# Kernel optimization log

Hardware: AMD Instinct MI355X
Metric: run time of the kernel (lower is better)

Reference implementation:

```python
import jax, jax.numpy as jnp
import numpy as np

EMB_DIM = 300
VOCAB_X = 50000
VOCAB_Y = 50000
LEN_X = 64
LEN_Y = 64
BATCH = 1024
PAD_ID = 0


def setup_inputs() -> dict:
    key = jax.random.key(0)
    k1, k2, k3, k4, k5, k6, k7 = jax.random.split(key, 7)
    initrange = 0.5 / EMB_DIM
    emb_x = jax.random.uniform(k1, (VOCAB_X, EMB_DIM), jnp.float32, -initrange, initrange)
    emb_y = jax.random.uniform(k2, (VOCAB_Y, EMB_DIM), jnp.float32, -initrange, initrange)
    # padding row zeroed as in init_emb
    emb_x = emb_x.at[PAD_ID].set(0.0)
    emb_y = emb_y.at[PAD_ID].set(0.0)
    return {
        "samp_hid": jax.random.normal(k3, (BATCH, EMB_DIM), jnp.float32),
        "batch_x": jax.random.randint(k4, (BATCH, LEN_X), 0, VOCAB_X, jnp.int64 if jax.config.jax_enable_x64 else jnp.int32),
        "batch_y": jax.random.randint(k5, (BATCH, LEN_Y), 0, VOCAB_Y, jnp.int64 if jax.config.jax_enable_x64 else jnp.int32),
        "emb_x": emb_x,
        "emb_y": emb_y,
        "bias_x": jax.random.uniform(k6, (VOCAB_X,), jnp.float32),
        "bias_y": jax.random.uniform(k7, (VOCAB_Y,), jnp.float32),
    }


def _cal_nll(z, tokens, emb, bias):
    # logits shared across all positions: [B, V]
    logits = z @ emb.T + bias
    logp = jax.nn.log_softmax(logits, axis=-1)            # compute log-softmax ONCE per row
    tok_logp = jnp.take_along_axis(logp, tokens, axis=1)  # [B, L] gather per-position targets
    mask = (tokens != PAD_ID).astype(logits.dtype)        # CrossEntropyLoss(ignore_index=0)
    return jnp.sum(-tok_logp * mask, axis=1)              # sum over positions -> [B]


def reference(samp_hid, batch_x, batch_y, emb_x, emb_y, bias_x, bias_y):
    nll_x = _cal_nll(samp_hid, batch_x, emb_x, bias_x)
    nll_y = _cal_nll(samp_hid, batch_y, emb_y, bias_y)
    return jnp.mean(nll_x + nll_y)
```

## Files before the change

kernel.cpp:

```cpp
#include <hip/hip_runtime.h>

#define V_VOCAB 50000
#define K_DIM   300
#define NROWS   1024
#define LEN     64
#define NBC     392
#define CGS     1568
#define KS      19

typedef __attribute__((ext_vector_type(8)))  short bf16x8;
typedef __attribute__((ext_vector_type(16))) float f32x16;

static __device__ __forceinline__ unsigned short f2bf(float f) {
    unsigned int u = __builtin_bit_cast(unsigned int, f);
    u = u + 0x7fffu + ((u >> 16) & 1u);
    return (unsigned short)(u >> 16);
}

static __device__ __forceinline__ f32x16 zero16() {
    f32x16 z;
#pragma unroll
    for (int i = 0; i < 16; ++i) z[i] = 0.0f;
    return z;
}

static __device__ __forceinline__ void gload_lds16(const void* g, void* l) {
    __builtin_amdgcn_global_load_lds((const __attribute__((address_space(1))) void*)g,
                                     (__attribute__((address_space(3))) void*)l, 16, 0, 0);
}

__global__ void zbf_kernel(const float* __restrict__ z, unsigned short* __restrict__ zbf) {
    int t = blockIdx.x * 256 + threadIdx.x;
    int l    = t & 63;
    int rest = t >> 6;
    int ks   = rest % KS;
    int rblk = rest / KS;
    int row  = rblk * 32 + (l & 31);
    int k0   = ks * 16 + (l >> 5) * 8;
    unsigned short o[8];
#pragma unroll
    for (int j = 0; j < 8; ++j) {
        int k = k0 + j;
        float v = (k < K_DIM) ? z[row * K_DIM + k] : ((k == K_DIM) ? 1.0f : 0.0f);
        o[j] = f2bf(v);
    }
    ushort4* p = (ushort4*)(zbf + (size_t)t * 8);
    p[0] = make_ushort4(o[0], o[1], o[2], o[3]);
    p[1] = make_ushort4(o[4], o[5], o[6], o[7]);
}

__launch_bounds__(256, 2)
__global__ void gemm_kernel(const unsigned short* __restrict__ zbf,
                            const float* __restrict__ emb_x,
                            const float* __restrict__ emb_y,
                            const float* __restrict__ bias_x,
                            const float* __restrict__ bias_y,
                            float* __restrict__ partial,
                            float* __restrict__ lsesum,
                            int accmode) {
    __shared__ unsigned short Zs[2][19456];

    const int tid  = threadIdx.x;
    const int lane = tid & 63;
    const int w    = tid >> 6;
    const int side = blockIdx.y;
    const int bc   = blockIdx.x;
    const float* eg = side ? emb_y : emb_x;
    const float* bg = side ? bias_y : bias_x;

    {
        const unsigned short* src = zbf;
#pragma unroll
        for (int i = 0; i < 10; ++i) {
            int q = w * 10 + i;
            if (q >= 38) q -= 8;
            gload_lds16(src + (size_t)q * 512 + lane * 8, &Zs[0][q * 512]);
        }
    }

    bf16x8 a[KS];
    {
        const int c  = bc * 128 + w * 32 + (lane & 31);
        const bool cv = (c < V_VOCAB);
        const float* erow = eg + (size_t)c * K_DIM;
        const int khi = (lane >> 5) * 8;
#pragma unroll
        for (int ks = 0; ks < KS; ++ks) {
            const int k0 = ks * 16 + khi;
            float f[8];
            if (k0 + 8 <= K_DIM) {
                float4 u  = cv ? *(const float4*)(erow + k0)     : make_float4(0, 0, 0, 0);
                float4 v2 = cv ? *(const float4*)(erow + k0 + 4) : make_float4(0, 0, 0, 0);
                f[0] = u.x;  f[1] = u.y;  f[2] = u.z;  f[3] = u.w;
                f[4] = v2.x; f[5] = v2.y; f[6] = v2.z; f[7] = v2.w;
            } else {
#pragma unroll
                for (int j = 0; j < 8; ++j) {
                    int k = k0 + j;
                    f[j] = (k < K_DIM) ? (cv ? erow[k] : 0.0f)
                         : (k == K_DIM ? (cv ? bg[c] : -3e38f) : 0.0f);
                }
            }
            bf16x8 t;
#pragma unroll
            for (int j = 0; j < 8; ++j) t[j] = (short)f2bf(f[j]);
            a[ks] = t;
        }
    }

    float* pout = partial + ((size_t)side * CGS + (size_t)bc * 4 + w) * NROWS;
    float* lout = lsesum + side * NROWS;

    int buf = 0;
    for (int p = 0; p < 16; ++p) {
        if (p < 15) {
            const unsigned short* src = zbf + (size_t)(p + 1) * 19456;
#pragma unroll
            for (int i = 0; i < 10; ++i) {
                int q = w * 10 + i;
                if (q >= 38) q -= 8;
                gload_lds16(src + (size_t)q * 512 + lane * 8, &Zs[buf ^ 1][q * 512]);
            }
            asm volatile("s_waitcnt vmcnt(10)" ::: "memory");
        } else {
            asm volatile("s_waitcnt vmcnt(0)" ::: "memory");
        }
        __builtin_amdgcn_s_barrier();
        __builtin_amdgcn_sched_barrier(0);

        const unsigned short* zb = &Zs[buf][0];
        f32x16 acc0 = zero16(), acc1 = zero16();
#pragma unroll
        for (int ks = 0; ks < KS; ++ks) {
            bf16x8 b0 = *(const bf16x8*)(zb + ((size_t)ks * 64 + lane) * 8);
            bf16x8 b1 = *(const bf16x8*)(zb + ((size_t)(KS + ks) * 64 + lane) * 8);
            acc0 = __builtin_amdgcn_mfma_f32_32x32x16_bf16(a[ks], b0, acc0, 0, 0, 0);
            acc1 = __builtin_amdgcn_mfma_f32_32x32x16_bf16(a[ks], b1, acc1, 0, 0, 0);
        }

        float s0 = 0.0f, s1 = 0.0f;
#pragma unroll
        for (int r = 0; r < 16; ++r) {
            s0 += __expf(acc0[r]);
            s1 += __expf(acc1[r]);
        }
        float t0 = s0 + __shfl_xor(s0, 32, 64);
        float t1 = s1 + __shfl_xor(s1, 32, 64);
        float val = (lane < 32) ? t0 : t1;
        if (accmode) atomicAdd(lout + p * 64 + lane, val);
        else         pout[p * 64 + lane] = val;

        __builtin_amdgcn_s_barrier();
        buf ^= 1;
    }
}

__global__ void lse_kernel(const float* __restrict__ partial, float* __restrict__ lse) {
    __shared__ float red[1024];
    int side = blockIdx.x >> 4;
    int mg   = blockIdx.x & 15;
    int m    = mg * 64 + (threadIdx.x & 63);
    int sg   = threadIdx.x >> 6;
    const float* p = partial + (size_t)side * CGS * NROWS;
    float s = 0.0f;
    for (int cg = sg; cg < CGS; cg += 16)
        s += p[(size_t)cg * NROWS + m];
    red[threadIdx.x] = s;
    __syncthreads();
    if (threadIdx.x < 64) {
        float t = 0.0f;
#pragma unroll
        for (int j = 0; j < 16; ++j) t += red[threadIdx.x + 64 * j];
        lse[side * NROWS + mg * 64 + threadIdx.x] = logf(t);
    }
}

__global__ void lse_log_kernel(float* __restrict__ lsesum) {
    int g = blockIdx.x * 1024 + threadIdx.x;
    if (g < 2 * NROWS) lsesum[g] = logf(lsesum[g]);
}

__global__ void gatherdot_kernel(const float* __restrict__ z,
                                 const int* __restrict__ tok_x, const int* __restrict__ tok_y,
                                 const float* __restrict__ emb_x, const float* __restrict__ emb_y,
                                 const float* __restrict__ bias_x, const float* __restrict__ bias_y,
                                 const float* __restrict__ lse, float* __restrict__ nllpart) {
    __shared__ float gs[304];
    const int b = blockIdx.x, side = blockIdx.y, tid = threadIdx.x;
    const int* tokp = (side ? tok_y : tok_x) + b * LEN;
    const float* eg = side ? emb_y : emb_x;
    if (tid < K_DIM) {
        float g0 = 0.0f, g1 = 0.0f, g2 = 0.0f, g3 = 0.0f;
#pragma unroll 4
        for (int pos = 0; pos < LEN; pos += 4) {
            int t0 = tokp[pos], t1 = tokp[pos + 1], t2 = tokp[pos + 2], t3 = tokp[pos + 3];
            if (t0) g0 += eg[(size_t)t0 * K_DIM + tid];
            if (t1) g1 += eg[(size_t)t1 * K_DIM + tid];
            if (t2) g2 += eg[(size_t)t2 * K_DIM + tid];
            if (t3) g3 += eg[(size_t)t3 * K_DIM + tid];
        }
        gs[tid] = (g0 + g1) + (g2 + g3);
    }
    __syncthreads();
    if (tid < 64) {
        const float* bg = side ? bias_y : bias_x;
        float dp = 0.0f;
#pragma unroll
        for (int i = 0; i < 5; ++i) {
            int d = tid + i * 64;
            if (d < K_DIM) dp += z[(size_t)b * K_DIM + d] * gs[d];
        }
        int t = tokp[tid];
        float bs = t ? bg[t] : 0.0f;
        float ct = t ? 1.0f : 0.0f;
#pragma unroll
        for (int off = 32; off > 0; off >>= 1) {
            dp += __shfl_xor(dp, off, 64);
            bs += __shfl_xor(bs, off, 64);
            ct += __shfl_xor(ct, off, 64);
        }
        if (tid == 0) nllpart[side * NROWS + b] = ct * lse[side * NROWS + b] - dp - bs;
    }
}

__global__ void finalize_kernel(const float* __restrict__ nllpart, float* __restrict__ out) {
    __shared__ float r16[16];
    int i = threadIdx.x;
    float v = nllpart[i] + nllpart[NROWS + i];
#pragma unroll
    for (int off = 32; off > 0; off >>= 1) v += __shfl_xor(v, off, 64);
    if ((i & 63) == 0) r16[i >> 6] = v;
    __syncthreads();
    if (i < 64) {
        float x = (i < 16) ? r16[i] : 0.0f;
#pragma unroll
        for (int off = 8; off > 0; off >>= 1) x += __shfl_xor(x, off, 64);
        if (i == 0) out[0] = x * (1.0f / 1024.0f);
    }
}

extern "C" void kernel_launch(void* const* d_in, const int* in_sizes, int n_in,
                              void* d_out, int out_size, void* d_ws, size_t ws_size,
                              hipStream_t stream) {
    const float* z      = (const float*)d_in[0];
    const int*   tok_x  = (const int*)d_in[1];
    const int*   tok_y  = (const int*)d_in[2];
    const float* emb_x  = (const float*)d_in[3];
    const float* emb_y  = (const float*)d_in[4];
    const float* bias_x = (const float*)d_in[5];
    const float* bias_y = (const float*)d_in[6];
    float* out = (float*)d_out;

    char* ws = (char*)d_ws;
    const size_t ZBF_B  = 622592;
    const size_t PART_B = (size_t)2 * CGS * NROWS * 4;
    const size_t need   = ZBF_B + PART_B + 8192 + 8192;

    unsigned short* zbf = (unsigned short*)ws;
    zbf_kernel<<<152, 256, 0, stream>>>(z, zbf);

    if (ws_size >= need) {
        float* partial = (float*)(ws + ZBF_B);
        float* lse     = (float*)(ws + ZBF_B + PART_B);
        float* nllpart = (float*)(ws + ZBF_B + PART_B + 8192);
        gemm_kernel<<<dim3(NBC, 2), 256, 0, stream>>>(zbf, emb_x, emb_y, bias_x, bias_y,
                                                      partial, lse , 0);
        lse_kernel<<<32, 1024, 0, stream>>>(partial, lse);
        gatherdot_kernel<<<dim3(NROWS, 2), 320, 0, stream>>>(z, tok_x, tok_y, emb_x, emb_y,
                                                             bias_x, bias_y, lse, nllpart);
        finalize_kernel<<<1, 1024, 0, stream>>>(nllpart, out);
    } else {
        float* lse     = (float*)(ws + ZBF_B);
        float* nllpart = (float*)(ws + ZBF_B + 8192);
        hipMemsetAsync(lse, 0, 8192, stream);
        gemm_kernel<<<dim3(NBC, 2), 256, 0, stream>>>(zbf, emb_x, emb_y, bias_x, bias_y,
                                                      nllpart , lse, 1);
        lse_log_kernel<<<2, 1024, 0, stream>>>(lse);
        gatherdot_kernel<<<dim3(NROWS, 2), 320, 0, stream>>>(z, tok_x, tok_y, emb_x, emb_y,
                                                             bias_x, bias_y, lse, nllpart);
        finalize_kernel<<<1, 1024, 0, stream>>>(nllpart, out);
    }
}
```

Before: 168.1 us.

## Give each wave two vocab tiles sharing B fragments, and use exp2

```diff
diff --git a/kernel.cpp b/kernel.cpp
--- a/kernel.cpp
+++ b/kernel.cpp
@@ -5,8 +5,10 @@
 #define NROWS   1024
 #define LEN     64
 #define NBC     392
-#define CGS     1568
+#define CGS     784
 #define KS      19
+#define PASSES  32
+#define LOG2E   1.44269504088896f
 
 typedef __attribute__((ext_vector_type(8)))  short bf16x8;
 typedef __attribute__((ext_vector_type(16))) float f32x16;
@@ -41,7 +43,8 @@
 #pragma unroll
     for (int j = 0; j < 8; ++j) {
         int k = k0 + j;
-        float v = (k < K_DIM) ? z[row * K_DIM + k] : ((k == K_DIM) ? 1.0f : 0.0f);
+        float v = (k < K_DIM) ? z[row * K_DIM + k] * LOG2E
+                              : ((k == K_DIM) ? LOG2E : 0.0f);
         o[j] = f2bf(v);
     }
     ushort4* p = (ushort4*)(zbf + (size_t)t * 8);
@@ -49,16 +52,17 @@
     p[1] = make_ushort4(o[4], o[5], o[6], o[7]);
 }
 
-__launch_bounds__(256, 2)
-__global__ void gemm_kernel(const unsigned short* __restrict__ zbf,
-                            const float* __restrict__ emb_x,
-                            const float* __restrict__ emb_y,
-                            const float* __restrict__ bias_x,
-                            const float* __restrict__ bias_y,
-                            float* __restrict__ partial,
-                            float* __restrict__ lsesum,
-                            int accmode) {
-    __shared__ unsigned short Zs[2][19456];
+__attribute__((amdgpu_waves_per_eu(2, 2)))
+__global__ void __launch_bounds__(128)
+gemm_kernel(const unsigned short* __restrict__ zbf,
+            const float* __restrict__ emb_x,
+            const float* __restrict__ emb_y,
+            const float* __restrict__ bias_x,
+            const float* __restrict__ bias_y,
+            float* __restrict__ partial,
+            float* __restrict__ lsesum,
+            int accmode) {
+    __shared__ unsigned short Zs[2][9728];
 
     const int tid  = threadIdx.x;
     const int lane = tid & 63;
@@ -73,14 +77,15 @@
 #pragma unroll
         for (int i = 0; i < 10; ++i) {
             int q = w * 10 + i;
-            if (q >= 38) q -= 8;
+            if (q > 18) q = 18;
             gload_lds16(src + (size_t)q * 512 + lane * 8, &Zs[0][q * 512]);
         }
     }
 
-    bf16x8 a[KS];
-    {
-        const int c  = bc * 128 + w * 32 + (lane & 31);
+    bf16x8 a0[KS], a1[KS];
+#pragma unroll
+    for (int cb = 0; cb < 2; ++cb) {
+        const int c  = bc * 128 + w * 64 + cb * 32 + (lane & 31);
         const bool cv = (c < V_VOCAB);
         const float* erow = eg + (size_t)c * K_DIM;
         const int khi = (lane >> 5) * 8;
@@ -104,21 +109,21 @@
             bf16x8 t;
 #pragma unroll
             for (int j = 0; j < 8; ++j) t[j] = (short)f2bf(f[j]);
-            a[ks] = t;
-        }
-    }
-
-    float* pout = partial + ((size_t)side * CGS + (size_t)bc * 4 + w) * NROWS;
+            if (cb == 0) a0[ks] = t; else a1[ks] = t;
+        }
+    }
+
+    float* pout = partial + ((size_t)side * CGS + (size_t)bc * 2 + w) * NROWS;
     float* lout = lsesum + side * NROWS;
 
     int buf = 0;
-    for (int p = 0; p < 16; ++p) {
-        if (p < 15) {
-            const unsigned short* src = zbf + (size_t)(p + 1) * 19456;
+    for (int p = 0; p < PASSES; ++p) {
+        if (p < PASSES - 1) {
+            const unsigned short* src = zbf + (size_t)(p + 1) * 9728;
 #pragma unroll
             for (int i = 0; i < 10; ++i) {
                 int q = w * 10 + i;
-                if (q >= 38) q -= 8;
+                if (q > 18) q = 18;
                 gload_lds16(src + (size_t)q * 512 + lane * 8, &Zs[buf ^ 1][q * 512]);
             }
             asm volatile("s_waitcnt vmcnt(10)" ::: "memory");
@@ -132,23 +137,21 @@
         f32x16 acc0 = zero16(), acc1 = zero16();
 #pragma unroll
         for (int ks = 0; ks < KS; ++ks) {
-            bf16x8 b0 = *(const bf16x8*)(zb + ((size_t)ks * 64 + lane) * 8);
-            bf16x8 b1 = *(const bf16x8*)(zb + ((size_t)(KS + ks) * 64 + lane) * 8);
-            acc0 = __builtin_amdgcn_mfma_f32_32x32x16_bf16(a[ks], b0, acc0, 0, 0, 0);
-            acc1 = __builtin_amdgcn_mfma_f32_32x32x16_bf16(a[ks], b1, acc1, 0, 0, 0);
+            bf16x8 b = *(const bf16x8*)(zb + ((size_t)ks * 64 + lane) * 8);
+            acc0 = __builtin_amdgcn_mfma_f32_32x32x16_bf16(a0[ks], b, acc0, 0, 0, 0);
+            acc1 = __builtin_amdgcn_mfma_f32_32x32x16_bf16(a1[ks], b, acc1, 0, 0, 0);
         }
 
         float s0 = 0.0f, s1 = 0.0f;
 #pragma unroll
         for (int r = 0; r < 16; ++r) {
-            s0 += __expf(acc0[r]);
-            s1 += __expf(acc1[r]);
-        }
-        float t0 = s0 + __shfl_xor(s0, 32, 64);
-        float t1 = s1 + __shfl_xor(s1, 32, 64);
-        float val = (lane < 32) ? t0 : t1;
-        if (accmode) atomicAdd(lout + p * 64 + lane, val);
-        else         pout[p * 64 + lane] = val;
+            s0 += exp2f(acc0[r]);
+            s1 += exp2f(acc1[r]);
+        }
+        float t = s0 + s1;
+        t += __shfl_xor(t, 32, 64);
+        if (accmode) { if (lane < 32) atomicAdd(lout + p * 32 + lane, t); }
+        else         { if (lane < 32) pout[p * 32 + lane] = t; }
 
         __builtin_amdgcn_s_barrier();
         buf ^= 1;
@@ -263,7 +266,7 @@
         float* partial = (float*)(ws + ZBF_B);
         float* lse     = (float*)(ws + ZBF_B + PART_B);
         float* nllpart = (float*)(ws + ZBF_B + PART_B + 8192);
-        gemm_kernel<<<dim3(NBC, 2), 256, 0, stream>>>(zbf, emb_x, emb_y, bias_x, bias_y,
+        gemm_kernel<<<dim3(NBC, 2), 128, 0, stream>>>(zbf, emb_x, emb_y, bias_x, bias_y,
                                                       partial, lse , 0);
         lse_kernel<<<32, 1024, 0, stream>>>(partial, lse);
         gatherdot_kernel<<<dim3(NROWS, 2), 320, 0, stream>>>(z, tok_x, tok_y, emb_x, emb_y,
@@ -273,7 +276,7 @@
         float* lse     = (float*)(ws + ZBF_B);
         float* nllpart = (float*)(ws + ZBF_B + 8192);
         hipMemsetAsync(lse, 0, 8192, stream);
-        gemm_kernel<<<dim3(NBC, 2), 256, 0, stream>>>(zbf, emb_x, emb_y, bias_x, bias_y,
+        gemm_kernel<<<dim3(NBC, 2), 128, 0, stream>>>(zbf, emb_x, emb_y, bias_x, bias_y,
                                                       nllpart , lse, 1);
         lse_log_kernel<<<2, 1024, 0, stream>>>(lse);
         gatherdot_kernel<<<dim3(NROWS, 2), 320, 0, stream>>>(z, tok_x, tok_y, emb_x, emb_y,
```

Measured after the change: 186.1 us. +10.7%, slower.
